# Performance work log

Hardware: AMD Instinct MI355X
Metric: run time of the kernel (lower is better)

The kernel has to match this reference:

```python
import jax, jax.numpy as jnp
import numpy as np

N_FEAT = 8   # node_features_count
E_FEAT = 4   # edge_features_count
NUM_IN = 2 * (N_FEAT + 2) + E_FEAT + 1   # 25
NUM_OUT = 2 * N_FEAT + E_FEAT           # 20
E = 1048576  # number of edges (batched)


def setup_inputs() -> dict:
    key = jax.random.key(0)
    ks = jax.random.split(key, 12)
    inp = {
        "r": jax.random.uniform(ks[0], (E,), dtype=jnp.float32),
        "a_data": jax.random.normal(ks[1], (E, N_FEAT), dtype=jnp.float32),
        "a_material": jax.random.normal(ks[2], (E,), dtype=jnp.float32),
        "a_influx": jax.random.normal(ks[3], (E,), dtype=jnp.float32),
        "b_data": jax.random.normal(ks[4], (E, N_FEAT), dtype=jnp.float32),
        "b_material": jax.random.normal(ks[5], (E,), dtype=jnp.float32),
        "b_influx": jax.random.normal(ks[6], (E,), dtype=jnp.float32),
        "e_data": jax.random.normal(ks[7], (E, E_FEAT), dtype=jnp.float32),
        # Linear params, init matching torch: weight ~ N(0, 0.1), bias = 0
        "W1": 0.1 * jax.random.normal(ks[8], (NUM_IN, NUM_IN), dtype=jnp.float32),
        "b1": jnp.zeros((NUM_IN,), dtype=jnp.float32),
        "W2": 0.1 * jax.random.normal(ks[9], (NUM_OUT, NUM_IN), dtype=jnp.float32),
        "b2": jnp.zeros((NUM_OUT,), dtype=jnp.float32),
    }
    return inp


def reference(r, a_data, a_material, a_influx, b_data, b_material, b_influx,
              e_data, W1, b1, W2, b2):
    # concat per-edge features: [E, NUM_IN]
    x = jnp.concatenate(
        [r[:, None], a_data, a_material[:, None], a_influx[:, None],
         b_data, b_material[:, None], b_influx[:, None], e_data], axis=1)
    x = jax.nn.relu(x @ W1.T + b1)            # [E, NUM_IN]
    x = jax.nn.relu(x @ W2.T + b2)            # [E, NUM_OUT]
    n = N_FEAT
    return (x[:, 0:n], x[:, n:2 * n], x[:, 2 * n:])
```

## Files before the change

kernel.cpp:

```cpp
#include <hip/hip_runtime.h>
#include <cstdint>

constexpr int N_FEAT  = 8;
constexpr int E_FEAT  = 4;
constexpr int NUM_IN  = 2 * (N_FEAT + 2) + E_FEAT + 1;
constexpr int NUM_OUT = 2 * N_FEAT + E_FEAT;

__global__ __launch_bounds__(256)
__attribute__((amdgpu_waves_per_eu(4, 4)))
void edge_mlp(
    const float* __restrict__ r,
    const float* __restrict__ a_data,
    const float* __restrict__ a_mat,
    const float* __restrict__ a_inf,
    const float* __restrict__ b_data,
    const float* __restrict__ b_mat,
    const float* __restrict__ b_inf,
    const float* __restrict__ e_data,
    const float* __restrict__ W1,
    const float* __restrict__ B1,
    const float* __restrict__ W2,
    const float* __restrict__ B2,
    float*       __restrict__ out,
    int E) {
  int e = blockIdx.x * blockDim.x + threadIdx.x;
  if (e >= E) return;

  const float4* a4 = reinterpret_cast<const float4*>(a_data) + 2 * (size_t)e;
  const float4* b4 = reinterpret_cast<const float4*>(b_data) + 2 * (size_t)e;
  float4 a0 = a4[0], a1 = a4[1];
  float4 b0 = b4[0], b1v = b4[1];
  float4 ev = reinterpret_cast<const float4*>(e_data)[e];

  float x[NUM_IN];
  x[0]  = r[e];
  x[1]  = a0.x; x[2]  = a0.y; x[3]  = a0.z; x[4]  = a0.w;
  x[5]  = a1.x; x[6]  = a1.y; x[7]  = a1.z; x[8]  = a1.w;
  x[9]  = a_mat[e];
  x[10] = a_inf[e];
  x[11] = b0.x; x[12] = b0.y; x[13] = b0.z; x[14] = b0.w;
  x[15] = b1v.x; x[16] = b1v.y; x[17] = b1v.z; x[18] = b1v.w;
  x[19] = b_mat[e];
  x[20] = b_inf[e];
  x[21] = ev.x; x[22] = ev.y; x[23] = ev.z; x[24] = ev.w;

  float h[NUM_IN];
#pragma unroll
  for (int j = 0; j < NUM_IN; ++j) {
    float acc = B1[j];
    const float* wr = W1 + j * NUM_IN;
#pragma unroll
    for (int k = 0; k < NUM_IN; ++k) acc = fmaf(wr[k], x[k], acc);
    h[j] = fmaxf(acc, 0.0f);
  }

  float y[NUM_OUT];
#pragma unroll
  for (int j = 0; j < NUM_OUT; ++j) {
    float acc = B2[j];
    const float* wr = W2 + j * NUM_IN;
#pragma unroll
    for (int k = 0; k < NUM_IN; ++k) acc = fmaf(wr[k], h[k], acc);
    y[j] = fmaxf(acc, 0.0f);
  }

  float4* o0 = reinterpret_cast<float4*>(out) + 2 * (size_t)e;
  o0[0] = make_float4(y[0], y[1], y[2],  y[3]);
  o0[1] = make_float4(y[4], y[5], y[6],  y[7]);
  float4* o1 = reinterpret_cast<float4*>(out + (size_t)8 * E) + 2 * (size_t)e;
  o1[0] = make_float4(y[8],  y[9],  y[10], y[11]);
  o1[1] = make_float4(y[12], y[13], y[14], y[15]);
  reinterpret_cast<float4*>(out + (size_t)16 * E)[e] =
      make_float4(y[16], y[17], y[18], y[19]);
}

extern "C" void kernel_launch(void* const* d_in, const int* in_sizes, int n_in,
                              void* d_out, int out_size, void* d_ws, size_t ws_size,
                              hipStream_t stream) {
  const float* r      = (const float*)d_in[0];
  const float* a_data = (const float*)d_in[1];
  const float* a_mat  = (const float*)d_in[2];
  const float* a_inf  = (const float*)d_in[3];
  const float* b_data = (const float*)d_in[4];
  const float* b_mat  = (const float*)d_in[5];
  const float* b_inf  = (const float*)d_in[6];
  const float* e_data = (const float*)d_in[7];
  const float* W1     = (const float*)d_in[8];
  const float* B1     = (const float*)d_in[9];
  const float* W2     = (const float*)d_in[10];
  const float* B2     = (const float*)d_in[11];
  int E = in_sizes[0];

  edge_mlp<<<(E + 255) / 256, 256, 0, stream>>>(
      r, a_data, a_mat, a_inf, b_data, b_mat, b_inf, e_data,
      W1, B1, W2, B2, (float*)d_out, E);
}
```

Before: 208.1 us.

## Compute edge MLP layers with fp16 MFMA using shared-memory staged tiles

```diff
diff --git a/kernel.cpp b/kernel.cpp
--- a/kernel.cpp
+++ b/kernel.cpp
@@ -5,9 +5,15 @@
 constexpr int E_FEAT  = 4;
 constexpr int NUM_IN  = 2 * (N_FEAT + 2) + E_FEAT + 1;
 constexpr int NUM_OUT = 2 * N_FEAT + E_FEAT;
+constexpr int BLK     = 256;
+constexpr int RS      = 40;
 
-__global__ __launch_bounds__(256)
-__attribute__((amdgpu_waves_per_eu(4, 4)))
+
+typedef _Float16 f16x8 __attribute__((ext_vector_type(8)));
+typedef float    f32x4 __attribute__((ext_vector_type(4)));
+
+__global__ __launch_bounds__(BLK)
+__attribute__((amdgpu_waves_per_eu(3, 4)))
 void edge_mlp(
     const float* __restrict__ r,
     const float* __restrict__ a_data,
@@ -23,55 +29,107 @@
     const float* __restrict__ B2,
     float*       __restrict__ out,
     int E) {
-  int e = blockIdx.x * blockDim.x + threadIdx.x;
-  if (e >= E) return;
+  __shared__ __align__(16) _Float16 sX[BLK * RS];
+  __shared__ __align__(16) _Float16 sW1[32 * 32];
+  __shared__ __align__(16) _Float16 sW2[32 * 32];
+  __shared__ float sB1[32];
+  __shared__ float sB2[32];
 
-  const float4* a4 = reinterpret_cast<const float4*>(a_data) + 2 * (size_t)e;
-  const float4* b4 = reinterpret_cast<const float4*>(b_data) + 2 * (size_t)e;
-  float4 a0 = a4[0], a1 = a4[1];
-  float4 b0 = b4[0], b1v = b4[1];
-  float4 ev = reinterpret_cast<const float4*>(e_data)[e];
+  const int tid = threadIdx.x;
 
-  float x[NUM_IN];
-  x[0]  = r[e];
-  x[1]  = a0.x; x[2]  = a0.y; x[3]  = a0.z; x[4]  = a0.w;
-  x[5]  = a1.x; x[6]  = a1.y; x[7]  = a1.z; x[8]  = a1.w;
-  x[9]  = a_mat[e];
-  x[10] = a_inf[e];
-  x[11] = b0.x; x[12] = b0.y; x[13] = b0.z; x[14] = b0.w;
-  x[15] = b1v.x; x[16] = b1v.y; x[17] = b1v.z; x[18] = b1v.w;
-  x[19] = b_mat[e];
-  x[20] = b_inf[e];
-  x[21] = ev.x; x[22] = ev.y; x[23] = ev.z; x[24] = ev.w;
-
-  float h[NUM_IN];
-#pragma unroll
-  for (int j = 0; j < NUM_IN; ++j) {
-    float acc = B1[j];
-    const float* wr = W1 + j * NUM_IN;
-#pragma unroll
-    for (int k = 0; k < NUM_IN; ++k) acc = fmaf(wr[k], x[k], acc);
-    h[j] = fmaxf(acc, 0.0f);
+  for (int i = tid; i < 1024; i += BLK) {
+    const int row = i >> 5, col = i & 31;
+    sW1[i] = (row < NUM_IN  && col < NUM_IN) ? (_Float16)W1[row * NUM_IN + col]
+                                             : (_Float16)0.f;
+    sW2[i] = (row < NUM_OUT && col < NUM_IN) ? (_Float16)W2[row * NUM_IN + col]
+                                             : (_Float16)0.f;
+  }
+  if (tid < 32) {
+    sB1[tid] = (tid < NUM_IN)  ? B1[tid] : 0.f;
+    sB2[tid] = (tid < NUM_OUT) ? B2[tid] : 0.f;
   }
 
-  float y[NUM_OUT];
+  const int ebase = blockIdx.x * BLK;
+  int eg = ebase + tid;
+  if (eg >= E) eg = E - 1;
+  const float4* a4 = reinterpret_cast<const float4*>(a_data) + 2 * (size_t)eg;
+  const float4* b4 = reinterpret_cast<const float4*>(b_data) + 2 * (size_t)eg;
+  const float4 a0 = a4[0], a1 = a4[1];
+  const float4 b0 = b4[0], b1v = b4[1];
+  const float4 ev = reinterpret_cast<const float4*>(e_data)[eg];
+  const float rv = r[eg], am = a_mat[eg], ai = a_inf[eg];
+  const float bm = b_mat[eg], bi = b_inf[eg];
+
+  f16x8 p0, p1, p2, p3;
+  p0[0] = (_Float16)rv;    p0[1] = (_Float16)a0.x;  p0[2] = (_Float16)a0.y;
+  p0[3] = (_Float16)a0.z;  p0[4] = (_Float16)a0.w;  p0[5] = (_Float16)a1.x;
+  p0[6] = (_Float16)a1.y;  p0[7] = (_Float16)a1.z;
+  p1[0] = (_Float16)a1.w;  p1[1] = (_Float16)am;    p1[2] = (_Float16)ai;
+  p1[3] = (_Float16)b0.x;  p1[4] = (_Float16)b0.y;  p1[5] = (_Float16)b0.z;
+  p1[6] = (_Float16)b0.w;  p1[7] = (_Float16)b1v.x;
+  p2[0] = (_Float16)b1v.y; p2[1] = (_Float16)b1v.z; p2[2] = (_Float16)b1v.w;
+  p2[3] = (_Float16)bm;    p2[4] = (_Float16)bi;    p2[5] = (_Float16)ev.x;
+  p2[6] = (_Float16)ev.y;  p2[7] = (_Float16)ev.z;
+  p3 = (f16x8)(_Float16)0.f;
+  p3[0] = (_Float16)ev.w;
+
+  _Float16* xrow = &sX[tid * RS];
+  *reinterpret_cast<f16x8*>(xrow + 0)  = p0;
+  *reinterpret_cast<f16x8*>(xrow + 8)  = p1;
+  *reinterpret_cast<f16x8*>(xrow + 16) = p2;
+  *reinterpret_cast<f16x8*>(xrow + 24) = p3;
+
+  __syncthreads();
+
+  const int lane = tid & 63;
+  const int lr   = lane & 15;
+  const int lk   = (lane >> 4) * 8;
+  const int rg   = (lane >> 4) * 4;
+  const int wid  = tid >> 6;
+
+  const f16x8 w1a = *reinterpret_cast<const f16x8*>(&sW1[lr * 32 + lk]);
+  const f16x8 w1b = *reinterpret_cast<const f16x8*>(&sW1[(16 + lr) * 32 + lk]);
+  const f16x8 w2a = *reinterpret_cast<const f16x8*>(&sW2[lr * 32 + lk]);
+  const f16x8 w2b = *reinterpret_cast<const f16x8*>(&sW2[(16 + lr) * 32 + lk]);
+  const float b1a = sB1[lr], b1b = sB1[16 + lr];
+  const float b2a = sB2[lr], b2b = sB2[16 + lr];
+
+  const size_t E8 = (size_t)E * 8;
+  float* yp0 = (lr < 8) ? (out + lr) : (out + E8 + (lr - 8));
+  float* yp1 = out + 2 * E8 + lr;
+
 #pragma unroll
-  for (int j = 0; j < NUM_OUT; ++j) {
-    float acc = B2[j];
-    const float* wr = W2 + j * NUM_IN;
+  for (int t = 0; t < 4; ++t) {
+    const int rb = wid * 64 + t * 16;
+
+    const f16x8 xa = *reinterpret_cast<const f16x8*>(&sX[(rb + lr) * RS + lk]);
+    f32x4 c0 = {b1a, b1a, b1a, b1a};
+    f32x4 c1 = {b1b, b1b, b1b, b1b};
+    c0 = __builtin_amdgcn_mfma_f32_16x16x32_f16(xa, w1a, c0, 0, 0, 0);
+    c1 = __builtin_amdgcn_mfma_f32_16x16x32_f16(xa, w1b, c1, 0, 0, 0);
+
 #pragma unroll
-    for (int k = 0; k < NUM_IN; ++k) acc = fmaf(wr[k], h[k], acc);
-    y[j] = fmaxf(acc, 0.0f);
+    for (int q = 0; q < 4; ++q) {
+      const int hr = rb + rg + q;
+      sX[hr * RS + lr]      = (_Float16)fmaxf(c0[q], 0.f);
+      sX[hr * RS + 16 + lr] = (_Float16)fmaxf(c1[q], 0.f);
+    }
+
+    const f16x8 ha = *reinterpret_cast<const f16x8*>(&sX[(rb + lr) * RS + lk]);
+    f32x4 d0 = {b2a, b2a, b2a, b2a};
+    f32x4 d1 = {b2b, b2b, b2b, b2b};
+    d0 = __builtin_amdgcn_mfma_f32_16x16x32_f16(ha, w2a, d0, 0, 0, 0);
+    d1 = __builtin_amdgcn_mfma_f32_16x16x32_f16(ha, w2b, d1, 0, 0, 0);
+
+#pragma unroll
+    for (int q = 0; q < 4; ++q) {
+      const int grow = ebase + rb + rg + q;
+      if (grow < E) {
+        yp0[(size_t)grow * 8] = fmaxf(d0[q], 0.f);
+        if (lr < 4) yp1[(size_t)grow * 4] = fmaxf(d1[q], 0.f);
+      }
+    }
   }
-
-  float4* o0 = reinterpret_cast<float4*>(out) + 2 * (size_t)e;
-  o0[0] = make_float4(y[0], y[1], y[2],  y[3]);
-  o0[1] = make_float4(y[4], y[5], y[6],  y[7]);
-  float4* o1 = reinterpret_cast<float4*>(out + (size_t)8 * E) + 2 * (size_t)e;
-  o1[0] = make_float4(y[8],  y[9],  y[10], y[11]);
-  o1[1] = make_float4(y[12], y[13], y[14], y[15]);
-  reinterpret_cast<float4*>(out + (size_t)16 * E)[e] =
-      make_float4(y[16], y[17], y[18], y[19]);
 }
 
 extern "C" void kernel_launch(void* const* d_in, const int* in_sizes, int n_in,
@@ -91,7 +149,7 @@
   const float* B2     = (const float*)d_in[11];
   int E = in_sizes[0];
 
-  edge_mlp<<<(E + 255) / 256, 256, 0, stream>>>(
+  edge_mlp<<<(E + BLK - 1) / BLK, BLK, 0, stream>>>(
       r, a_data, a_mat, a_inf, b_data, b_mat, b_inf, e_data,
       W1, B1, W2, B2, (float*)d_out, E);
 }
```

Measured after the change: 197.2 us. 1.05x faster.
